# Kernel optimization log

Hardware: AMD Instinct MI355X
Metric: run time of the kernel (lower is better)

Reference implementation:

```python
import jax, jax.numpy as jnp
from jax import lax
import numpy as np

B, T, U, V = 4, 300, 64, 1024
FEAT, H, L = 80, 512, 3            # encoder: 3-layer bidirectional LSTM
HD = 512                           # decoder hidden (1 layer)
ENC_OUT = DEC_OUT = 512
INNER = 512
DMAX = max(FEAT, 2 * H)            # padded input dim for stacked encoder weights
NEG = -1e30


def setup_inputs() -> dict:
    key = jax.random.key(0)
    ks = jax.random.split(key, 20)
    s = 1.0 / np.sqrt(H)
    u = lambda k, shp: jax.random.uniform(k, shp, jnp.float32, -s, s)
    inputs = jax.random.normal(ks[0], (B, T, FEAT), jnp.float32)
    inputs_length = jax.random.randint(ks[1], (B,), T // 2, T + 1, jnp.int32)
    targets = jax.random.randint(ks[2], (B, U), 1, V, jnp.int32)
    targets_length = jax.random.randint(ks[3], (B,), U // 2, U + 1, jnp.int32)
    enc_Wih = u(ks[4], (L, 2, 4 * H, DMAX))   # layer0 uses first FEAT cols
    enc_Whh = u(ks[5], (L, 2, 4 * H, H))
    enc_b = u(ks[6], (L, 2, 4 * H))           # b_ih + b_hh fused
    enc_proj_W = u(ks[7], (ENC_OUT, 2 * H))
    enc_proj_b = u(ks[8], (ENC_OUT,))
    dec_emb = u(ks[9], (V, HD)).at[0].set(0.0)  # padding_idx=0
    dec_Wih = u(ks[10], (4 * HD, HD))
    dec_Whh = u(ks[11], (4 * HD, HD))
    dec_b = u(ks[12], (4 * HD,))
    dec_proj_W = u(ks[13], (DEC_OUT, HD))
    dec_proj_b = u(ks[14], (DEC_OUT,))
    j_fwd_W = u(ks[15], (INNER, ENC_OUT + DEC_OUT))
    j_fwd_b = u(ks[16], (INNER,))
    j_proj_W = u(ks[17], (V, INNER))
    j_proj_b = u(ks[18], (V,))
    return dict(inputs=inputs, inputs_length=inputs_length, targets=targets,
                targets_length=targets_length, enc_Wih=enc_Wih, enc_Whh=enc_Whh,
                enc_b=enc_b, enc_proj_W=enc_proj_W, enc_proj_b=enc_proj_b,
                dec_emb=dec_emb, dec_Wih=dec_Wih, dec_Whh=dec_Whh, dec_b=dec_b,
                dec_proj_W=dec_proj_W, dec_proj_b=dec_proj_b, j_fwd_W=j_fwd_W,
                j_fwd_b=j_fwd_b, j_proj_W=j_proj_W, j_proj_b=j_proj_b)


def lstm_layer(x, Wih, Whh, b):
    # x: [B, T, Din]; torch gate order (i, f, g, o)
    Bb = x.shape[0]
    Hh = Whh.shape[1]
    xg = jnp.einsum('btd,gd->btg', x, Wih) + b  # precompute input projections

    def step(carry, xt):
        h, c = carry
        g = xt + h @ Whh.T
        i, f, gg, o = jnp.split(g, 4, axis=-1)
        c = jax.nn.sigmoid(f) * c + jax.nn.sigmoid(i) * jnp.tanh(gg)
        h = jax.nn.sigmoid(o) * jnp.tanh(c)
        return (h, c), h

    z = jnp.zeros((Bb, Hh), x.dtype)
    _, hs = lax.scan(step, (z, z), xg.transpose(1, 0, 2))
    return hs.transpose(1, 0, 2)


def reverse_padded(x, lengths):
    # reverse each sequence within its valid length (packed-sequence semantics)
    t = jnp.arange(x.shape[1])
    idx = jnp.where(t[None] < lengths[:, None], lengths[:, None] - 1 - t[None], t[None])
    return jnp.take_along_axis(x, idx[:, :, None], axis=1)


def rnnt_loss(log_probs, targets, T_len, U_len):
    # log_probs: [B, T, U+1, V], blank = 0
    Bb, Tt, U1, _ = log_probs.shape
    Uu = U1 - 1
    blank = log_probs[..., 0]                                   # [B,T,U+1]
    idx = jnp.broadcast_to(targets[:, None, :, None], (Bb, Tt, Uu, 1))
    lab = jnp.take_along_axis(log_probs[:, :, :Uu, :], idx, axis=3)[..., 0]  # [B,T,U]

    def row_update(a, c):
        # solves x[u] = logaddexp(a[u], x[u-1] + c[u-1]) via log-space cumsum
        C = jnp.concatenate([jnp.zeros((Bb, 1), a.dtype), jnp.cumsum(c, axis=1)], axis=1)
        return C + lax.cumlogsumexp(a - C, axis=1)

    a0 = jnp.full((Bb, U1), NEG, log_probs.dtype).at[:, 0].set(0.0)
    alpha0 = row_update(a0, lab[:, 0])

    def step(alpha_prev, xs):
        bl_prev, lab_t = xs
        alpha = row_update(alpha_prev + bl_prev, lab_t)
        return alpha, alpha

    xs = (blank[:, :-1].transpose(1, 0, 2), lab[:, 1:].transpose(1, 0, 2))
    _, alphas = lax.scan(step, alpha0, xs)                      # [T-1,B,U+1]
    alphas = jnp.concatenate([alpha0[None], alphas], axis=0)    # [T,B,U+1]
    b_idx = jnp.arange(Bb)
    ll = alphas[T_len - 1, b_idx, U_len] + blank[b_idx, T_len - 1, U_len]
    return -jnp.mean(ll)


def reference(inputs, inputs_length, targets, targets_length, enc_Wih, enc_Whh,
              enc_b, enc_proj_W, enc_proj_b, dec_emb, dec_Wih, dec_Whh, dec_b,
              dec_proj_W, dec_proj_b, j_fwd_W, j_fwd_b, j_proj_W, j_proj_b):
    # ---- encoder: stacked bi-LSTM + projection ----
    mask = (jnp.arange(T)[None] < inputs_length[:, None])[..., None].astype(inputs.dtype)
    x = inputs
    for l in range(L):
        Din = x.shape[-1]
        fwd = lstm_layer(x, enc_Wih[l, 0, :, :Din], enc_Whh[l, 0], enc_b[l, 0])
        bwd = reverse_padded(
            lstm_layer(reverse_padded(x, inputs_length), enc_Wih[l, 1, :, :Din],
                       enc_Whh[l, 1], enc_b[l, 1]), inputs_length)
        x = jnp.concatenate([fwd, bwd], axis=-1) * mask
    enc = jnp.einsum('bth,oh->bto', x, enc_proj_W) + enc_proj_b  # [B,T,ENC_OUT]

    # ---- decoder: blank-prepended targets -> embed -> LSTM -> projection ----
    dec_in = jnp.pad(targets, ((0, 0), (1, 0)))                  # [B,U+1]
    demb = dec_emb[dec_in]
    dmask = (jnp.arange(U + 1)[None] < (targets_length + 1)[:, None])[..., None].astype(demb.dtype)
    dh = lstm_layer(demb, dec_Wih, dec_Whh, dec_b) * dmask
    dec = jnp.einsum('buh,oh->buo', dh, dec_proj_W) + dec_proj_b  # [B,U+1,DEC_OUT]

    # ---- joint: broadcast T x (U+1), split concat-matmul into two matmuls ----
    We, Wd = j_fwd_W[:, :ENC_OUT], j_fwd_W[:, ENC_OUT:]
    hj = jnp.tanh(jnp.einsum('bto,io->bti', enc, We)[:, :, None, :]
                  + jnp.einsum('buo,io->bui', dec, Wd)[:, None, :, :] + j_fwd_b)
    logits = jnp.einsum('btui,vi->btuv', hj, j_proj_W) + j_proj_b  # [B,T,U+1,V]
    log_probs = jax.nn.log_softmax(logits, axis=-1)

    return rnnt_loss(log_probs, targets, inputs_length, targets_length)
```

## Files before the change

### kernel.cpp

```cpp
#include <hip/hip_runtime.h>
#include <hip/hip_bf16.h>

#define B_ 4
#define T_ 300
#define U_ 64
#define U1_ 65
#define V_ 1024
#define H_ 512
#define G4_ 2048
#define NW_ 32
#define RPB_ (T_ * U1_)
#define NTILE_ 305
#define RPAD_ 19520

typedef __hip_bfloat16 bf16;
typedef unsigned long long u64;
typedef __attribute__((ext_vector_type(8))) short short8;
typedef __attribute__((ext_vector_type(4))) float floatx4;

__device__ __forceinline__ float b2f(bf16 x) { return __bfloat162float(x); }
__device__ __forceinline__ bf16 f2b(float x) { return __float2bfloat16(x); }
__device__ __forceinline__ short bf16bits(float x) {
  bf16 h = __float2bfloat16(x);
  return *reinterpret_cast<short*>(&h);
}
__device__ __forceinline__ short8 pack8(float4 a, float4 b) {
  short8 p;
  p[0] = bf16bits(a.x); p[1] = bf16bits(a.y); p[2] = bf16bits(a.z); p[3] = bf16bits(a.w);
  p[4] = bf16bits(b.x); p[5] = bf16bits(b.y); p[6] = bf16bits(b.z); p[7] = bf16bits(b.w);
  return p;
}
__device__ __forceinline__ float sigm_(float x) { return 1.f / (1.f + __expf(-x)); }
__device__ __forceinline__ float tanh_(float x) { return 1.f - 2.f / (1.f + __expf(2.f * x)); }
__device__ __forceinline__ float lae_(float x, float y) {
  float m = fmaxf(x, y);
  float n = fminf(x, y);
  return m + __logf(1.f + __expf(n - m));
}

__global__ void prep_kernel(const float* __restrict__ in, bf16* __restrict__ x0) {
  int i = blockIdx.x * 256 + threadIdx.x;
  if (i < B_ * T_ * 128) {
    int k = i & 127;
    int row = i >> 7;
    float v = (k < 80) ? in[row * 80 + k] : 0.f;
    x0[(size_t)row * 1024 + k] = f2b(v);
  }
}

__global__ void embed_kernel(const float* __restrict__ emb, const int* __restrict__ tgt,
                             bf16* __restrict__ demb) {
  int i = blockIdx.x * 256 + threadIdx.x;
  if (i >= B_ * U1_ * 512) return;
  int k = i & 511;
  int bu = i >> 9;
  int u = bu % U1_, b = bu / U1_;
  int id = (u == 0) ? 0 : tgt[b * U_ + u - 1];
  demb[i] = f2b(emb[(size_t)id * 512 + k]);
}

__global__ __launch_bounds__(256) void gemm_kernel(
    const bf16* __restrict__ A, int lda,
    const float* __restrict__ W, int ldw,
    const float* __restrict__ bias,
    void* __restrict__ Cout, int out_f32, int ldc,
    int M, int K) {
  __shared__ __align__(16) bf16 As[64][72];
  __shared__ __align__(16) bf16 Bs[64][72];
  int m0 = blockIdx.x * 64, n0 = blockIdx.y * 64;
  int tid = threadIdx.x, w = tid >> 6, l = tid & 63;
  int l4 = l & 15, lq = l >> 4;
  floatx4 acc[4];
#pragma unroll
  for (int nt = 0; nt < 4; ++nt) acc[nt] = (floatx4){0.f, 0.f, 0.f, 0.f};
  for (int k0 = 0; k0 < K; k0 += 64) {
    __syncthreads();
#pragma unroll
    for (int q = 0; q < 2; ++q) {
      int cc = tid + q * 256;
      int r = cc >> 3, kc = (cc & 7) * 8;
      short8 va = {0, 0, 0, 0, 0, 0, 0, 0};
      int gm = m0 + r;
      if (gm < M) va = *(const short8*)(A + (size_t)gm * lda + k0 + kc);
      *(short8*)(&As[r][kc]) = va;
      const float* wp = W + (size_t)(n0 + r) * ldw + k0 + kc;
      float4 w0 = *(const float4*)(wp);
      float4 w1 = *(const float4*)(wp + 4);
      *(short8*)(&Bs[r][kc]) = pack8(w0, w1);
    }
    __syncthreads();
#pragma unroll
    for (int kk = 0; kk < 64; kk += 32) {
      short8 a = *(const short8*)(&As[w * 16 + l4][kk + lq * 8]);
#pragma unroll
      for (int nt = 0; nt < 4; ++nt) {
        short8 bb = *(const short8*)(&Bs[nt * 16 + l4][kk + lq * 8]);
        acc[nt] = __builtin_amdgcn_mfma_f32_16x16x32_bf16(a, bb, acc[nt], 0, 0, 0);
      }
    }
  }
#pragma unroll
  for (int nt = 0; nt < 4; ++nt) {
    int col = n0 + nt * 16 + l4;
    float bv = bias ? bias[col] : 0.f;
#pragma unroll
    for (int r = 0; r < 4; ++r) {
      int row = m0 + w * 16 + lq * 4 + r;
      if (row < M) {
        float v = acc[nt][r] + bv;
        if (out_f32) ((float*)Cout)[(size_t)row * ldc + col] = v;
        else ((bf16*)Cout)[(size_t)row * ldc + col] = f2b(v);
      }
    }
  }
}

__global__ __launch_bounds__(256, 1) void scan_kernel(
    const float* __restrict__ xg,
    const float* __restrict__ whh,
    const int* __restrict__ len_raw, int len_add,
    int Tmax, int bwd_mask,
    bf16* __restrict__ out, int out_stride,
    int dec_d,
    const float* __restrict__ xg2, const float* __restrict__ whh2,
    const int* __restrict__ len_raw2, int len_add2,
    int Tmax2, bf16* __restrict__ out2, int out_stride2,
    u64* __restrict__ hpk) {
  int w = blockIdx.x, d = blockIdx.y;
  int tid = threadIdx.x;
  bool isdec = (d == dec_d);
  const float* xg_d = isdec ? xg2 : xg + (size_t)d * B_ * Tmax * G4_;
  const float* whh_d = isdec ? whh2 : whh + (size_t)d * G4_ * H_;
  const int* lens = isdec ? len_raw2 : len_raw;
  int ladd = isdec ? len_add2 : len_add;
  int tmax = isdec ? Tmax2 : Tmax;
  bf16* outp = isdec ? out2 : out;
  int ostride = isdec ? out_stride2 : out_stride;
  int ocol = isdec ? 0 : d * H_;
  bool bwd = isdec ? false : ((bwd_mask >> d) & 1);
  u64* hp = hpk + (size_t)d * 4096;

  int sub = tid >> 6;
  int l = tid & 63;
  int col = l & 15;
  int lq = l >> 4;
  int gate = col & 3;
  int dloc = col >> 2;
  int dim = w * 16 + sub * 4 + dloc;
  int grow = gate * H_ + dim;
  int sb = l & 12;

  __shared__ int len_s[4];
  __shared__ __align__(16) bf16 h_lds[2][16][512];

  if (tid < 4) len_s[tid] = lens[tid] + ladd;
  {
    unsigned* hz = (unsigned*)&h_lds[0][0][0];
#pragma unroll
    for (int i = 0; i < 32; ++i) hz[tid + i * 256] = 0u;
  }

  short8 bfr[16];
  {
    const float* wp = whh_d + (size_t)grow * H_ + lq * 8;
#pragma unroll
    for (int ks2 = 0; ks2 < 16; ++ks2) {
      float4 w0 = *(const float4*)(wp + ks2 * 32);
      float4 w1 = *(const float4*)(wp + ks2 * 32 + 4);
      bfr[ks2] = pack8(w0, w1);
    }
  }
  __syncthreads();
  int smax = max(max(len_s[0], len_s[1]), max(len_s[2], len_s[3]));

  int D0 = sub * 128 + 2 * l;
  float cst = 0.f;
  char* hbase = (char*)&h_lds[0][0][0];
  unsigned rsw = (unsigned)((l & 7) << 4);
  unsigned rbyte = (unsigned)((l & 15) * 1024 + lq * 16);

  for (int s = 0; s < smax; ++s) {
    int p = s & 1;
    char* pl = hbase + p * 16384;
    float xv[4];
    if (l < 16) {
#pragma unroll
      for (int b = 0; b < 4; ++b) {
        int lb = len_s[b];
        int rt = bwd ? (lb - 1 - s) : s;
        if (s >= lb) rt = 0;
        xv[b] = xg_d[((size_t)b * tmax + rt) * G4_ + grow];
      }
    }
    if (s > 0) {
      const u64* src = hp + ((s - 1) & 1) * 2048;
      u64 v[8];
      for (;;) {
        bool ok = true;
#pragma unroll
        for (int b = 0; b < 4; ++b) {
          v[2 * b] = __hip_atomic_load(src + b * 512 + D0, __ATOMIC_RELAXED,
                                       __HIP_MEMORY_SCOPE_AGENT);
          v[2 * b + 1] = __hip_atomic_load(src + b * 512 + D0 + 1, __ATOMIC_RELAXED,
                                           __HIP_MEMORY_SCOPE_AGENT);
          ok &= ((int)(unsigned)v[2 * b] == s) & ((int)(unsigned)v[2 * b + 1] == s);
        }
        if (__all(ok)) break;
      }
      unsigned cb = (unsigned)(D0 * 2);
#pragma unroll
      for (int b = 0; b < 4; ++b) {
        float f0 = __uint_as_float((unsigned)(v[2 * b] >> 32));
        float f1 = __uint_as_float((unsigned)(v[2 * b + 1] >> 32));
        bf16 h0 = f2b(f0), h1 = f2b(f1);
        float r0 = f0 - b2f(h0), r1 = f1 - b2f(h1);
        bf16 e0 = f2b(r0), e1 = f2b(r1);
        unsigned hi = (unsigned)*(unsigned short*)&h0 |
                      ((unsigned)*(unsigned short*)&h1 << 16);
        unsigned lo = (unsigned)*(unsigned short*)&e0 |
                      ((unsigned)*(unsigned short*)&e1 << 16);
        *(unsigned*)(pl + (((unsigned)(b * 1024) + cb) ^ (unsigned)(b << 4))) = hi;
        *(unsigned*)(pl + (((unsigned)((b + 4) * 1024) + cb) ^ (unsigned)((b + 4) << 4))) = lo;
      }
    }
    __syncthreads();
    floatx4 acc = (floatx4){0.f, 0.f, 0.f, 0.f};
#pragma unroll
    for (int ks2 = 0; ks2 < 16; ++ks2) {
      short8 a = *(const short8*)(pl + ((rbyte + (unsigned)(ks2 * 64)) ^ rsw));
      acc = __builtin_amdgcn_mfma_f32_16x16x32_bf16(a, bfr[ks2], acc, 0, 0, 0);
    }
    float hout = 0.f;
#pragma unroll
    for (int r = 0; r < 4; ++r) {
      float v2 = acc[r] + __shfl(acc[r], col + 16, 64);
      if (l < 16) v2 += xv[r];
      float gi = __shfl(v2, sb + 0, 64);
      float gf = __shfl(v2, sb + 1, 64);
      float gg = __shfl(v2, sb + 2, 64);
      float go = __shfl(v2, sb + 3, 64);
      if (l < 16 && (l & 3) == r && s < len_s[r]) {
        cst = sigm_(gf) * cst + sigm_(gi) * tanh_(gg);
        hout = sigm_(go) * tanh_(cst);
      }
    }
    if (l < 16) {
      int b = l & 3;
      u64 pkt = ((u64)__float_as_uint(hout) << 32) | (unsigned)(s + 1);
      __hip_atomic_store(hp + p * 2048 + b * 512 + dim, pkt,
                         __ATOMIC_RELAXED, __HIP_MEMORY_SCOPE_AGENT);
      if (s < len_s[b]) {
        int t = bwd ? (len_s[b] - 1 - s) : s;
        outp[((size_t)b * tmax + t) * ostride + ocol + dim] = f2b(hout);
      }
    }
  }
}

__global__ __launch_bounds__(256) void joint_kernel(
    const float* __restrict__ ea, const float* __restrict__ da,
    const float* __restrict__ Wp, const float* __restrict__ pb,
    const int* __restrict__ targets,
    float* __restrict__ blankraw, float* __restrict__ labraw,
    float* __restrict__ jstats) {
  __shared__ __align__(16) bf16 As[64][72];
  __shared__ __align__(16) bf16 Bs[256][72];
  __shared__ float bias_s[256];
  __shared__ int tgt_s[64];
  __shared__ float pstat[64][2][2];

  int tid = threadIdx.x;
  int tile = blockIdx.x, cb = blockIdx.y, b = blockIdx.z;
  int r0 = tile * 64;

  bias_s[tid & 255] = pb[cb * 256 + (tid & 255)];
  if (tid < 64) {
    int r = r0 + tid;
    int u = r % U1_;
    tgt_s[tid] = (r < RPB_ && u < U_) ? targets[b * U_ + u] : -1;
  }
  int si = tid >> 2;
  int sseg = (tid & 3) * 16;
  int sr = r0 + si;
  bool svalid = sr < RPB_;
  int st = svalid ? sr / U1_ : 0;
  int su = svalid ? sr % U1_ : 0;
  const float* ep = ea + ((size_t)(b * T_ + st)) * 512 + sseg;
  const float* dp = da + ((size_t)(b * U1_ + su)) * 512 + sseg;

  int wid = tid >> 6, l = tid & 63;
  int wm = wid >> 1, wn = wid & 1;
  int l4 = l & 15, lq = l >> 4;

  floatx4 acc[2][8];
#pragma unroll
  for (int ms = 0; ms < 2; ++ms)
#pragma unroll
    for (int nt = 0; nt < 8; ++nt) acc[ms][nt] = (floatx4){0.f, 0.f, 0.f, 0.f};

  for (int k0 = 0; k0 < 512; k0 += 64) {
    __syncthreads();
    {
      const float* e = ep + k0;
      const float* d = dp + k0;
#pragma unroll
      for (int h = 0; h < 2; ++h) {
        float4 e0 = *(const float4*)(e + h * 8);
        float4 e1 = *(const float4*)(e + h * 8 + 4);
        float4 d0 = *(const float4*)(d + h * 8);
        float4 d1 = *(const float4*)(d + h * 8 + 4);
        short8 pk = {0, 0, 0, 0, 0, 0, 0, 0};
        if (svalid) {
          pk[0] = bf16bits(tanh_(e0.x + d0.x));
          pk[1] = bf16bits(tanh_(e0.y + d0.y));
          pk[2] = bf16bits(tanh_(e0.z + d0.z));
          pk[3] = bf16bits(tanh_(e0.w + d0.w));
          pk[4] = bf16bits(tanh_(e1.x + d1.x));
          pk[5] = bf16bits(tanh_(e1.y + d1.y));
          pk[6] = bf16bits(tanh_(e1.z + d1.z));
          pk[7] = bf16bits(tanh_(e1.w + d1.w));
        }
        *(short8*)(&As[si][sseg + h * 8]) = pk;
      }
    }
#pragma unroll
    for (int q = 0; q < 8; ++q) {
      int cc = tid + q * 256;
      int r = cc >> 3, kc = (cc & 7) * 8;
      const float* wp = Wp + (size_t)(cb * 256 + r) * 512 + k0 + kc;
      float4 w0 = *(const float4*)(wp);
      float4 w1 = *(const float4*)(wp + 4);
      *(short8*)(&Bs[r][kc]) = pack8(w0, w1);
    }
    __syncthreads();
#pragma unroll
    for (int kk = 0; kk < 64; kk += 32) {
      short8 af[2], bf8[8];
#pragma unroll
      for (int ms = 0; ms < 2; ++ms)
        af[ms] = *(const short8*)(&As[wm * 32 + ms * 16 + l4][kk + lq * 8]);
#pragma unroll
      for (int nt = 0; nt < 8; ++nt)
        bf8[nt] = *(const short8*)(&Bs[wn * 128 + nt * 16 + l4][kk + lq * 8]);
#pragma unroll
      for (int ms = 0; ms < 2; ++ms)
#pragma unroll
        for (int nt = 0; nt < 8; ++nt)
          acc[ms][nt] = __builtin_amdgcn_mfma_f32_16x16x32_bf16(af[ms], bf8[nt], acc[ms][nt], 0, 0, 0);
    }
  }
#pragma unroll
  for (int ms = 0; ms < 2; ++ms) {
#pragma unroll
    for (int r = 0; r < 4; ++r) {
      int i = wm * 32 + ms * 16 + lq * 4 + r;
      int grow = r0 + i;
      bool valid = grow < RPB_;
      int tg = tgt_s[i];
      float v[8];
      float mx = -1e30f;
#pragma unroll
      for (int nt = 0; nt < 8; ++nt) {
        int colc = wn * 128 + nt * 16 + l4;
        float x = acc[ms][nt][r] + bias_s[colc];
        v[nt] = x;
        mx = fmaxf(mx, x);
        int gcol = cb * 256 + colc;
        if (valid) {
          if (gcol == 0) blankraw[(size_t)b * RPB_ + grow] = x;
          if (gcol == tg) labraw[(size_t)b * RPB_ + grow] = x;
        }
      }
#pragma unroll
      for (int dd = 1; dd < 16; dd <<= 1) mx = fmaxf(mx, __shfl_xor(mx, dd, 64));
      float se = 0.f;
#pragma unroll
      for (int nt = 0; nt < 8; ++nt) se += __expf(v[nt] - mx);
#pragma unroll
      for (int dd = 1; dd < 16; dd <<= 1) se += __shfl_xor(se, dd, 64);
      if (l4 == 0) { pstat[i][wn][0] = mx; pstat[i][wn][1] = se; }
    }
  }
  __syncthreads();
  if (tid < 64) {
    float ma = pstat[tid][0][0], sa = pstat[tid][0][1];
    float mb = pstat[tid][1][0], sb = pstat[tid][1][1];
    float mc = fmaxf(ma, mb);
    float sc = sa * __expf(ma - mc) + sb * __expf(mb - mc);
    size_t o = (((size_t)b * RPAD_ + r0 + tid) * 4 + cb) * 2;
    jstats[o] = mc;
    jstats[o + 1] = sc;
  }
}

__global__ void finalize_kernel(const float* __restrict__ jstats,
                                float* __restrict__ blank, float* __restrict__ lab) {
  int g = blockIdx.x * 256 + threadIdx.x;
  if (g >= B_ * RPB_) return;
  int b = g / RPB_, r = g % RPB_;
  const float* st = jstats + ((size_t)b * RPAD_ + r) * 8;
  float M = fmaxf(fmaxf(st[0], st[2]), fmaxf(st[4], st[6]));
  float s = st[1] * __expf(st[0] - M) + st[3] * __expf(st[2] - M) +
            st[5] * __expf(st[4] - M) + st[7] * __expf(st[6] - M);
  float lse = M + __logf(s);
  blank[g] -= lse;
  if ((r % U1_) < U_) lab[g] -= lse;
}

__global__ void loss_kernel(const float* __restrict__ blank, const float* __restrict__ lab,
                            const int* __restrict__ Tl, const int* __restrict__ Ul,
                            float* __restrict__ outp) {
  int b = threadIdx.x >> 6;
  int l = threadIdx.x & 63;
  int TL = Tl[b], UL = Ul[b];
  float alpha_l = 0.f, alpha0 = 0.f;
  for (int t = 0; t < TL; ++t) {
    float a_u0, a_l1;
    if (t == 0) { a_u0 = 0.f; a_l1 = -1e30f; }
    else {
      const float* bl = blank + ((size_t)b * T_ + (t - 1)) * U1_;
      a_u0 = alpha0 + bl[0];
      a_l1 = alpha_l + bl[l + 1];
    }
    const float* lb = lab + ((size_t)b * T_ + t) * U1_;
    float C = lb[l];
#pragma unroll
    for (int dd = 1; dd < 64; dd <<= 1) {
      float o = __shfl_up(C, dd, 64);
      if (l >= dd) C += o;
    }
    float S = a_l1 - C;
#pragma unroll
    for (int dd = 1; dd < 64; dd <<= 1) {
      float o = __shfl_up(S, dd, 64);
      if (l >= dd) S = lae_(S, o);
    }
    alpha_l = C + lae_(a_u0, S);
    alpha0 = a_u0;
  }
  float av = (UL == 0) ? alpha0 : __shfl(alpha_l, UL - 1, 64);
  float ll = av + blank[((size_t)b * T_ + (TL - 1)) * U1_ + UL];
  __shared__ float lls[4];
  if (l == 0) lls[b] = ll;
  __syncthreads();
  if (threadIdx.x == 0) outp[0] = -0.25f * (lls[0] + lls[1] + lls[2] + lls[3]);
}

static constexpr size_t OFF_XG = 0;
static constexpr size_t OFF_XA = OFF_XG + (size_t)2 * B_ * T_ * G4_ * 4;
static constexpr size_t OFF_XB = OFF_XA + (size_t)B_ * T_ * 1024 * 2;
static constexpr size_t OFF_ENC = OFF_XB + (size_t)B_ * T_ * 1024 * 2;
static constexpr size_t OFF_EA = OFF_ENC + (size_t)B_ * T_ * 512 * 2;
static constexpr size_t OFF_DEMB = OFF_EA + (size_t)B_ * T_ * 512 * 4;
static constexpr size_t OFF_DXG = OFF_DEMB + (size_t)B_ * U1_ * 512 * 2;
static constexpr size_t OFF_DH = OFF_DXG + (size_t)B_ * U1_ * G4_ * 4;
static constexpr size_t OFF_DEC = OFF_DH + (size_t)B_ * U1_ * 512 * 2;
static constexpr size_t OFF_DA = OFF_DEC + (size_t)B_ * U1_ * 512 * 2;
static constexpr size_t OFF_BL = OFF_DA + (size_t)B_ * U1_ * 512 * 4;
static constexpr size_t OFF_LAB = OFF_BL + (size_t)B_ * T_ * U1_ * 4;
static constexpr size_t OFF_HPK = OFF_LAB + (size_t)B_ * T_ * U1_ * 4;
static constexpr size_t OFF_JST = OFF_HPK + (size_t)7 * 4096 * 8;

extern "C" void kernel_launch(void* const* d_in, const int* in_sizes, int n_in,
                              void* d_out, int out_size, void* d_ws, size_t ws_size,
                              hipStream_t stream) {
  (void)in_sizes; (void)n_in; (void)out_size; (void)ws_size;
  const float* inputs = (const float*)d_in[0];
  const int* inputs_length = (const int*)d_in[1];
  const int* targets = (const int*)d_in[2];
  const int* targets_length = (const int*)d_in[3];
  const float* enc_Wih = (const float*)d_in[4];
  const float* enc_Whh = (const float*)d_in[5];
  const float* enc_b = (const float*)d_in[6];
  const float* enc_proj_W = (const float*)d_in[7];
  const float* enc_proj_b = (const float*)d_in[8];
  const float* dec_emb = (const float*)d_in[9];
  const float* dec_Wih = (const float*)d_in[10];
  const float* dec_Whh = (const float*)d_in[11];
  const float* dec_b = (const float*)d_in[12];
  const float* dec_proj_W = (const float*)d_in[13];
  const float* dec_proj_b = (const float*)d_in[14];
  const float* j_fwd_W = (const float*)d_in[15];
  const float* j_fwd_b = (const float*)d_in[16];
  const float* j_proj_W = (const float*)d_in[17];
  const float* j_proj_b = (const float*)d_in[18];

  char* ws = (char*)d_ws;
  float* xg = (float*)(ws + OFF_XG);
  bf16* xa = (bf16*)(ws + OFF_XA);
  bf16* xb = (bf16*)(ws + OFF_XB);
  bf16* encb = (bf16*)(ws + OFF_ENC);
  float* eab = (float*)(ws + OFF_EA);
  bf16* demb = (bf16*)(ws + OFF_DEMB);
  float* dxg = (float*)(ws + OFF_DXG);
  bf16* dh = (bf16*)(ws + OFF_DH);
  bf16* decb = (bf16*)(ws + OFF_DEC);
  float* dab = (float*)(ws + OFF_DA);
  float* blank = (float*)(ws + OFF_BL);
  float* lab = (float*)(ws + OFF_LAB);
  u64* hpk = (u64*)(ws + OFF_HPK);
  float* jstats = (float*)(ws + OFF_JST);

  prep_kernel<<<600, 256, 0, stream>>>(inputs, xa);
  embed_kernel<<<520, 256, 0, stream>>>(dec_emb, targets, demb);

  gemm_kernel<<<dim3(5, 32), 256, 0, stream>>>(demb, 512, dec_Wih, 512, dec_b,
                                               dxg, 1, G4_, B_ * U1_, 512);
  for (int dd = 0; dd < 2; ++dd) {
    gemm_kernel<<<dim3(19, 32), 256, 0, stream>>>(
        xa, 1024, enc_Wih + (size_t)dd * G4_ * 1024, 1024, enc_b + (size_t)dd * G4_,
        xg + (size_t)dd * B_ * T_ * G4_, 1, G4_, B_ * T_, 128);
  }
  scan_kernel<<<dim3(NW_, 3), 256, 0, stream>>>(
      xg, enc_Whh, inputs_length, 0, T_, 2, xb, 1024,
      2, dxg, dec_Whh, targets_length, 1, U1_, dh, 512,
      hpk);

  gemm_kernel<<<dim3(5, 8), 256, 0, stream>>>(dh, 512, dec_proj_W, 512, dec_proj_b,
                                              decb, 0, 512, B_ * U1_, 512);
  gemm_kernel<<<dim3(5, 8), 256, 0, stream>>>(decb, 512, j_fwd_W + 512, 1024, j_fwd_b,
                                              dab, 1, 512, B_ * U1_, 512);

  bf16* xcur = xb;
  for (int lyr = 1; lyr < 3; ++lyr) {
    bf16* xnext = (xcur == xa) ? xb : xa;
    for (int dd = 0; dd < 2; ++dd) {
      gemm_kernel<<<dim3(19, 32), 256, 0, stream>>>(
          xcur, 1024,
          enc_Wih + (size_t)(lyr * 2 + dd) * G4_ * 1024, 1024,
          enc_b + (size_t)(lyr * 2 + dd) * G4_,
          xg + (size_t)dd * B_ * T_ * G4_, 1, G4_, B_ * T_, 1024);
    }
    scan_kernel<<<dim3(NW_, 2), 256, 0, stream>>>(
        xg, enc_Whh + (size_t)lyr * 2 * G4_ * H_,
        inputs_length, 0, T_, 2, xnext, 1024,
        -1, dxg, dec_Whh, targets_length, 1, U1_, dh, 512,
        hpk + (size_t)(3 + 2 * (lyr - 1)) * 4096);
    xcur = xnext;
  }
  gemm_kernel<<<dim3(19, 8), 256, 0, stream>>>(xcur, 1024, enc_proj_W, 1024, enc_proj_b,
                                               encb, 0, 512, B_ * T_, 1024);
  gemm_kernel<<<dim3(19, 8), 256, 0, stream>>>(encb, 512, j_fwd_W, 1024, (const float*)nullptr,
                                               eab, 1, 512, B_ * T_, 512);

  joint_kernel<<<dim3(NTILE_, 4, B_), 256, 0, stream>>>(eab, dab, j_proj_W, j_proj_b, targets,
                                                        blank, lab, jstats);
  finalize_kernel<<<(B_ * RPB_ + 255) / 256, 256, 0, stream>>>(jstats, blank, lab);
  loss_kernel<<<1, 256, 0, stream>>>(blank, lab, inputs_length, targets_length, (float*)d_out);
}
```

Measured before the change: 3.512 ms.

## Use XCD-local fast polling path for LSTM scan cross-block handoff

The scan kernel's grid is reshaped to 8 x NW so that all blocks of one direction land on the same XCD under round-robin dispatch. Each hidden-state packet is stored twice: once with sc0 to a fast, L2-local buffer and once with sc0 sc1 to a system-coherent buffer. Waiters poll the fast buffer with vectorized dwordx4 loads and fall back to the slow buffer after a bounded number of tries. The change also prefetches the next step's input gates before the barrier, splits the MFMA chain into two accumulators, and adds a kernel that zeroes both buffers. The fast path depends on the assumed block-to-XCD placement, and the fallback guards correctness if that assumption fails.

```diff
diff --git a/kernel.cpp b/kernel.cpp
--- a/kernel.cpp
+++ b/kernel.cpp
@@ -12,11 +12,13 @@
 #define RPB_ (T_ * U1_)
 #define NTILE_ 305
 #define RPAD_ 19520
+#define FASTK_ 128
 
 typedef __hip_bfloat16 bf16;
 typedef unsigned long long u64;
 typedef __attribute__((ext_vector_type(8))) short short8;
 typedef __attribute__((ext_vector_type(4))) float floatx4;
+typedef __attribute__((ext_vector_type(4))) unsigned int uintx4;
 
 __device__ __forceinline__ float b2f(bf16 x) { return __bfloat162float(x); }
 __device__ __forceinline__ bf16 f2b(float x) { return __float2bfloat16(x); }
@@ -36,6 +38,40 @@
   float m = fmaxf(x, y);
   float n = fminf(x, y);
   return m + __logf(1.f + __expf(n - m));
+}
+
+__device__ __forceinline__ void poll4x4(const u64* a0, bool slow,
+                                        uintx4& q0, uintx4& q1,
+                                        uintx4& q2, uintx4& q3) {
+  const u64* a1 = a0 + 512;
+  const u64* a2 = a0 + 1024;
+  const u64* a3 = a0 + 1536;
+  if (!slow) {
+    asm volatile(
+        "global_load_dwordx4 %0, %4, off sc0\n\t"
+        "global_load_dwordx4 %1, %5, off sc0\n\t"
+        "global_load_dwordx4 %2, %6, off sc0\n\t"
+        "global_load_dwordx4 %3, %7, off sc0\n\t"
+        "s_waitcnt vmcnt(0)"
+        : "=&v"(q0), "=&v"(q1), "=&v"(q2), "=&v"(q3)
+        : "v"(a0), "v"(a1), "v"(a2), "v"(a3)
+        : "memory");
+  } else {
+    asm volatile(
+        "global_load_dwordx4 %0, %4, off sc0 sc1\n\t"
+        "global_load_dwordx4 %1, %5, off sc0 sc1\n\t"
+        "global_load_dwordx4 %2, %6, off sc0 sc1\n\t"
+        "global_load_dwordx4 %3, %7, off sc0 sc1\n\t"
+        "s_waitcnt vmcnt(0)"
+        : "=&v"(q0), "=&v"(q1), "=&v"(q2), "=&v"(q3)
+        : "v"(a0), "v"(a1), "v"(a2), "v"(a3)
+        : "memory");
+  }
+}
+
+__global__ void zero_hpk_kernel(u64* __restrict__ a, u64* __restrict__ b) {
+  int i = blockIdx.x * 256 + threadIdx.x;
+  if (i < 7 * 4096) { a[i] = 0ull; b[i] = 0ull; }
 }
 
 __global__ void prep_kernel(const float* __restrict__ in, bf16* __restrict__ x0) {
@@ -116,6 +152,7 @@
 }
 
 __global__ __launch_bounds__(256, 1) void scan_kernel(
+    int ndir,
     const float* __restrict__ xg,
     const float* __restrict__ whh,
     const int* __restrict__ len_raw, int len_add,
@@ -125,8 +162,9 @@
     const float* __restrict__ xg2, const float* __restrict__ whh2,
     const int* __restrict__ len_raw2, int len_add2,
     int Tmax2, bf16* __restrict__ out2, int out_stride2,
-    u64* __restrict__ hpk) {
-  int w = blockIdx.x, d = blockIdx.y;
+    u64* __restrict__ hpkS, u64* __restrict__ hpkF) {
+  int d = blockIdx.x, w = blockIdx.y;
+  if (d >= ndir) return;
   int tid = threadIdx.x;
   bool isdec = (d == dec_d);
   const float* xg_d = isdec ? xg2 : xg + (size_t)d * B_ * Tmax * G4_;
@@ -138,7 +176,8 @@
   int ostride = isdec ? out_stride2 : out_stride;
   int ocol = isdec ? 0 : d * H_;
   bool bwd = isdec ? false : ((bwd_mask >> d) & 1);
-  u64* hp = hpk + (size_t)d * 4096;
+  u64* hpS = hpkS + (size_t)d * 4096;
+  u64* hpF = hpkF + (size_t)d * 4096;
 
   int sub = tid >> 6;
   int l = tid & 63;
@@ -179,39 +218,41 @@
   unsigned rsw = (unsigned)((l & 7) << 4);
   unsigned rbyte = (unsigned)((l & 15) * 1024 + lq * 16);
 
+  bool slowp = false;
+
+  float xv[4];
+  if (l < 16) {
+#pragma unroll
+    for (int b = 0; b < 4; ++b) {
+      int lb = len_s[b];
+      int rt = bwd ? (lb - 1) : 0;
+      xv[b] = xg_d[((size_t)b * tmax + rt) * G4_ + grow];
+    }
+  }
+
   for (int s = 0; s < smax; ++s) {
     int p = s & 1;
     char* pl = hbase + p * 16384;
-    float xv[4];
-    if (l < 16) {
+    if (s > 0) {
+      unsigned ss = (unsigned)s;
+      const u64* srcS = hpS + ((s - 1) & 1) * 2048 + D0;
+      const u64* srcF = hpF + ((s - 1) & 1) * 2048 + D0;
+      uintx4 q0, q1, q2, q3;
+      int it = 0;
+      for (;;) {
+        poll4x4(slowp ? srcS : srcF, slowp, q0, q1, q2, q3);
+        bool ok = (q0[0] == ss) & (q0[2] == ss) & (q1[0] == ss) & (q1[2] == ss) &
+                  (q2[0] == ss) & (q2[2] == ss) & (q3[0] == ss) & (q3[2] == ss);
+        if (__all(ok)) break;
+        if (!slowp && ++it > FASTK_) slowp = true;
+      }
+      unsigned cb = (unsigned)(D0 * 2);
+      unsigned pay0[4] = {q0[1], q1[1], q2[1], q3[1]};
+      unsigned pay1[4] = {q0[3], q1[3], q2[3], q3[3]};
 #pragma unroll
       for (int b = 0; b < 4; ++b) {
-        int lb = len_s[b];
-        int rt = bwd ? (lb - 1 - s) : s;
-        if (s >= lb) rt = 0;
-        xv[b] = xg_d[((size_t)b * tmax + rt) * G4_ + grow];
-      }
-    }
-    if (s > 0) {
-      const u64* src = hp + ((s - 1) & 1) * 2048;
-      u64 v[8];
-      for (;;) {
-        bool ok = true;
-#pragma unroll
-        for (int b = 0; b < 4; ++b) {
-          v[2 * b] = __hip_atomic_load(src + b * 512 + D0, __ATOMIC_RELAXED,
-                                       __HIP_MEMORY_SCOPE_AGENT);
-          v[2 * b + 1] = __hip_atomic_load(src + b * 512 + D0 + 1, __ATOMIC_RELAXED,
-                                           __HIP_MEMORY_SCOPE_AGENT);
-          ok &= ((int)(unsigned)v[2 * b] == s) & ((int)(unsigned)v[2 * b + 1] == s);
-        }
-        if (__all(ok)) break;
-      }
-      unsigned cb = (unsigned)(D0 * 2);
-#pragma unroll
-      for (int b = 0; b < 4; ++b) {
-        float f0 = __uint_as_float((unsigned)(v[2 * b] >> 32));
-        float f1 = __uint_as_float((unsigned)(v[2 * b + 1] >> 32));
+        float f0 = __uint_as_float(pay0[b]);
+        float f1 = __uint_as_float(pay1[b]);
         bf16 h0 = f2b(f0), h1 = f2b(f1);
         float r0 = f0 - b2f(h0), r1 = f1 - b2f(h1);
         bf16 e0 = f2b(r0), e1 = f2b(r1);
@@ -223,13 +264,28 @@
         *(unsigned*)(pl + (((unsigned)((b + 4) * 1024) + cb) ^ (unsigned)((b + 4) << 4))) = lo;
       }
     }
+    float xvn[4];
+    if (l < 16) {
+      int sn = s + 1;
+#pragma unroll
+      for (int b = 0; b < 4; ++b) {
+        int lb = len_s[b];
+        int rt = bwd ? (lb - 1 - sn) : sn;
+        if (sn >= lb) rt = 0;
+        xvn[b] = xg_d[((size_t)b * tmax + rt) * G4_ + grow];
+      }
+    }
     __syncthreads();
-    floatx4 acc = (floatx4){0.f, 0.f, 0.f, 0.f};
-#pragma unroll
-    for (int ks2 = 0; ks2 < 16; ++ks2) {
-      short8 a = *(const short8*)(pl + ((rbyte + (unsigned)(ks2 * 64)) ^ rsw));
-      acc = __builtin_amdgcn_mfma_f32_16x16x32_bf16(a, bfr[ks2], acc, 0, 0, 0);
-    }
+    floatx4 accA = (floatx4){0.f, 0.f, 0.f, 0.f};
+    floatx4 accB = (floatx4){0.f, 0.f, 0.f, 0.f};
+#pragma unroll
+    for (int k2 = 0; k2 < 16; k2 += 2) {
+      short8 a0 = *(const short8*)(pl + ((rbyte + (unsigned)(k2 * 64)) ^ rsw));
+      short8 a1 = *(const short8*)(pl + ((rbyte + (unsigned)((k2 + 1) * 64)) ^ rsw));
+      accA = __builtin_amdgcn_mfma_f32_16x16x32_bf16(a0, bfr[k2], accA, 0, 0, 0);
+      accB = __builtin_amdgcn_mfma_f32_16x16x32_bf16(a1, bfr[k2 + 1], accB, 0, 0, 0);
+    }
+    floatx4 acc = accA + accB;
     float hout = 0.f;
 #pragma unroll
     for (int r = 0; r < 4; ++r) {
@@ -247,13 +303,19 @@
     if (l < 16) {
       int b = l & 3;
       u64 pkt = ((u64)__float_as_uint(hout) << 32) | (unsigned)(s + 1);
-      __hip_atomic_store(hp + p * 2048 + b * 512 + dim, pkt,
-                         __ATOMIC_RELAXED, __HIP_MEMORY_SCOPE_AGENT);
+      u64* paF = hpF + p * 2048 + b * 512 + dim;
+      u64* paS = hpS + p * 2048 + b * 512 + dim;
+      asm volatile("global_store_dwordx2 %0, %1, off sc0" ::"v"(paF), "v"(pkt)
+                   : "memory");
+      asm volatile("global_store_dwordx2 %0, %1, off sc0 sc1" ::"v"(paS), "v"(pkt)
+                   : "memory");
       if (s < len_s[b]) {
         int t = bwd ? (len_s[b] - 1 - s) : s;
         outp[((size_t)b * tmax + t) * ostride + ocol + dim] = f2b(hout);
       }
     }
+#pragma unroll
+    for (int b = 0; b < 4; ++b) xv[b] = xvn[b];
   }
 }
 
@@ -460,6 +522,7 @@
 static constexpr size_t OFF_LAB = OFF_BL + (size_t)B_ * T_ * U1_ * 4;
 static constexpr size_t OFF_HPK = OFF_LAB + (size_t)B_ * T_ * U1_ * 4;
 static constexpr size_t OFF_JST = OFF_HPK + (size_t)7 * 4096 * 8;
+static constexpr size_t OFF_FPK = OFF_JST + (size_t)B_ * RPAD_ * 4 * 2 * 4;
 
 extern "C" void kernel_launch(void* const* d_in, const int* in_sizes, int n_in,
                               void* d_out, int out_size, void* d_ws, size_t ws_size,
@@ -498,9 +561,11 @@
   float* dab = (float*)(ws + OFF_DA);
   float* blank = (float*)(ws + OFF_BL);
   float* lab = (float*)(ws + OFF_LAB);
-  u64* hpk = (u64*)(ws + OFF_HPK);
+  u64* hpkS = (u64*)(ws + OFF_HPK);
+  u64* hpkF = (u64*)(ws + OFF_FPK);
   float* jstats = (float*)(ws + OFF_JST);
 
+  zero_hpk_kernel<<<112, 256, 0, stream>>>(hpkS, hpkF);
   prep_kernel<<<600, 256, 0, stream>>>(inputs, xa);
   embed_kernel<<<520, 256, 0, stream>>>(dec_emb, targets, demb);
 
@@ -511,10 +576,10 @@
         xa, 1024, enc_Wih + (size_t)dd * G4_ * 1024, 1024, enc_b + (size_t)dd * G4_,
         xg + (size_t)dd * B_ * T_ * G4_, 1, G4_, B_ * T_, 128);
   }
-  scan_kernel<<<dim3(NW_, 3), 256, 0, stream>>>(
-      xg, enc_Whh, inputs_length, 0, T_, 2, xb, 1024,
+  scan_kernel<<<dim3(8, NW_), 256, 0, stream>>>(
+      3, xg, enc_Whh, inputs_length, 0, T_, 2, xb, 1024,
       2, dxg, dec_Whh, targets_length, 1, U1_, dh, 512,
-      hpk);
+      hpkS, hpkF);
 
   gemm_kernel<<<dim3(5, 8), 256, 0, stream>>>(dh, 512, dec_proj_W, 512, dec_proj_b,
                                               decb, 0, 512, B_ * U1_, 512);
@@ -531,11 +596,12 @@
           enc_b + (size_t)(lyr * 2 + dd) * G4_,
           xg + (size_t)dd * B_ * T_ * G4_, 1, G4_, B_ * T_, 1024);
     }
-    scan_kernel<<<dim3(NW_, 2), 256, 0, stream>>>(
-        xg, enc_Whh + (size_t)lyr * 2 * G4_ * H_,
+    scan_kernel<<<dim3(8, NW_), 256, 0, stream>>>(
+        2, xg, enc_Whh + (size_t)lyr * 2 * G4_ * H_,
         inputs_length, 0, T_, 2, xnext, 1024,
         -1, dxg, dec_Whh, targets_length, 1, U1_, dh, 512,
-        hpk + (size_t)(3 + 2 * (lyr - 1)) * 4096);
+        hpkS + (size_t)(3 + 2 * (lyr - 1)) * 4096,
+        hpkF + (size_t)(3 + 2 * (lyr - 1)) * 4096);
     xcur = xnext;
   }
   gemm_kernel<<<dim3(19, 8), 256, 0, stream>>>(xcur, 1024, enc_proj_W, 1024, enc_proj_b,
```

Result: no change. 3.539 ms (+0.8%).
